# Performance work log

Measured on AMD Instinct MI355X. Metric: run time of the kernel, lower is better.

The kernel has to match this reference:

```python
import jax, jax.numpy as jnp
import numpy as np

N_NODES = 40000
N_EDGES = 640000
D_IN = 128
D_OUT = 128
ALPHA = 0.5   # real-valued complex alpha from init
Q = 0.25      # magnetic potential parameter


def setup_inputs() -> dict:
    key = jax.random.key(0)
    k = jax.random.split(key, 6)
    x = jax.random.normal(k[0], (N_NODES, D_IN), dtype=jnp.float32)
    edge_index = jax.random.randint(k[1], (2, N_EDGES), 0, N_NODES, dtype=jnp.int32)
    W1 = jax.random.normal(k[2], (D_IN, D_OUT), dtype=jnp.float32) * 0.05
    b1 = jax.random.normal(k[3], (D_OUT,), dtype=jnp.float32) * 0.05
    W2 = jax.random.normal(k[4], (D_IN, D_OUT), dtype=jnp.float32) * 0.05
    b2 = jax.random.normal(k[5], (D_OUT,), dtype=jnp.float32) * 0.05
    return {"x": x, "edge_index": edge_index, "W1": W1, "b1": b1, "W2": W2, "b2": b2}


def _magnet_spmm(x, edge_index, q):
    """y = H @ x where H = D_s^{-1/2} (A_s * exp(i*2*pi*q*(A - A^T))) D_s^{-1/2},
    A_s = 0.5*(A + A^T). Returns (y_real, y_imag); x is real (zero imag part)."""
    n = x.shape[0]
    row, col = edge_index[0], edge_index[1]
    e = row.shape[0]
    # detect whether the reverse edge (col,row) exists in the edge set
    keys = row * n + col
    rkeys = col * n + row
    sk = jnp.sort(keys)
    pos = jnp.searchsorted(sk, rkeys)
    has_rev = (pos < e) & (sk[jnp.clip(pos, 0, e - 1)] == rkeys)
    # symmetrize: each directed edge contributes 0.5 in both directions.
    # forward copy carries phase sign +1, reversed copy sign -1; phase is 0
    # when both directions exist (A - A^T = 0 there).
    r_all = jnp.concatenate([row, col])          # [2E]
    c_all = jnp.concatenate([col, row])
    sign = jnp.concatenate([jnp.ones((e,), x.dtype), -jnp.ones((e,), x.dtype)])
    hr = jnp.concatenate([has_rev, has_rev]).astype(x.dtype)
    theta = (2.0 * np.pi * q) * sign * (1.0 - hr)
    half = jnp.asarray(0.5, x.dtype)
    # symmetrized degree: deg[u] = sum_v A_s[u,v]
    deg = jax.ops.segment_sum(jnp.full((2 * e,), 0.5, x.dtype), r_all, num_segments=n)
    dinv = jnp.where(deg > 0, 1.0 / jnp.sqrt(deg), 0.0)
    scale = half * dinv[r_all] * dinv[c_all]
    val_re = scale * jnp.cos(theta)
    val_im = scale * jnp.sin(theta)
    xg = x[c_all]                                # [2E, D] gather
    y_re = jax.ops.segment_sum(val_re[:, None] * xg, r_all, num_segments=n)
    y_im = jax.ops.segment_sum(val_im[:, None] * xg, r_all, num_segments=n)
    return y_re, y_im


def reference(x, edge_index, W1, b1, W2, b2):
    y_re, y_im = _magnet_spmm(x, edge_index, Q)
    # alpha * lin1(y) + (1-alpha) * lin2(y), applied to real and imag parts
    out_re = ALPHA * (y_re @ W1 + b1) + (1.0 - ALPHA) * (y_re @ W2 + b2)
    out_im = ALPHA * (y_im @ W1 + b1) + (1.0 - ALPHA) * (y_im @ W2 + b2)
    return jnp.concatenate([out_re, out_im], axis=1)  # [N, 2*D_OUT]
```

## Files before the change

### kernel.cpp

```cpp
#include <hip/hip_runtime.h>
#include <math.h>

#define N_NODES 40000
#define D 128
#define NEDGE 640000
#define CAP 80

__device__ __forceinline__ unsigned short bf16rn(float f) {
    unsigned u = __float_as_uint(f);
    unsigned r = u + 0x7FFFu + ((u >> 16) & 1u);
    return (unsigned short)(r >> 16);
}

__global__ void init_kernel(int* __restrict__ cursor,
                            const float* __restrict__ W1, const float* __restrict__ b1,
                            const float* __restrict__ W2, const float* __restrict__ b2,
                            float* __restrict__ Wc, float* __restrict__ bc,
                            const float* __restrict__ x, unsigned short* __restrict__ xb) {
    int i = blockIdx.x * blockDim.x + threadIdx.x;
    int stride = gridDim.x * blockDim.x;
    for (int t = i; t < N_NODES; t += stride) cursor[t] = 0;
    for (int t = i; t < D * D; t += stride) Wc[t] = 0.5f * (W1[t] + W2[t]);
    if (i < D) bc[i] = 0.5f * (b1[i] + b2[i]);
    if (xb) {
        for (int t = i; t < N_NODES * D / 4; t += stride) {
            float4 v = ((const float4*)x)[t];
            ushort4 o;
            o.x = bf16rn(v.x); o.y = bf16rn(v.y); o.z = bf16rn(v.z); o.w = bf16rn(v.w);
            ((ushort4*)xb)[t] = o;
        }
    }
}

__global__ void expand_kernel(const int* __restrict__ row, const int* __restrict__ col,
                              int* __restrict__ cursor, unsigned* __restrict__ entries) {
    int e = blockIdx.x * blockDim.x + threadIdx.x;
    if (e >= NEDGE) return;
    int r = row[e], c = col[e];
    int p1 = atomicAdd(&cursor[r], 1);
    if (p1 < CAP) entries[(size_t)r * CAP + p1] = (unsigned)c;
    int p2 = atomicAdd(&cursor[c], 1);
    if (p2 < CAP) entries[(size_t)c * CAP + p2] = (unsigned)r | 0x10000u;
}

template <int USE_BF16>
__global__ __launch_bounds__(256) void fused_kernel(
    const float* __restrict__ x, const unsigned short* __restrict__ xb,
    const unsigned* __restrict__ entries, const int* __restrict__ cursor,
    const float* __restrict__ Wc, const float* __restrict__ bc,
    float* __restrict__ out) {
    __shared__ unsigned rawlds[4][2][CAP];
    __shared__ uint4 slds[4][2][CAP];
    __shared__ float ylds[8][260];

    int tid = threadIdx.x;
    int wave = tid >> 6, half = (tid >> 5) & 1, l = tid & 31;
    int n = wave * 2 + half;
    int u = blockIdx.x * 8 + n;

    int cnt = cursor[u];
    int m = min(cnt, CAP);
    float dinv_u = (cnt > 0) ? rsqrtf(0.5f * (float)cnt) : 0.f;
    const unsigned* eb = entries + (size_t)u * CAP;

    for (int idx = l; idx < m; idx += 32) rawlds[wave][half][idx] = eb[idx];
    __builtin_amdgcn_wave_barrier();

    for (int idx = l; idx < m; idx += 32) {
        unsigned e = rawlds[wave][half][idx];
        unsigned src = e & 0xFFFFu;
        unsigned dir = (e >> 16) & 1u;
        unsigned tgt = src | ((dir ^ 1u) << 16);
        bool rev = false;
        for (int j = 0; j < m; ++j)
            rev |= (rawlds[wave][half][j] == tgt);
        int cs = cursor[src];
        float s = 0.5f * dinv_u * rsqrtf(0.5f * (float)max(cs, 1));
        float sre = 0.f, sim = 0.f;
        if (rev) sre = s;
        else sim = dir ? -s : s;
        slds[wave][half][idx] = make_uint4(src, __float_as_uint(sre),
                                           __float_as_uint(sim), 0u);
    }
    __builtin_amdgcn_wave_barrier();

    float4 accre = make_float4(0.f, 0.f, 0.f, 0.f);
    float4 accim = make_float4(0.f, 0.f, 0.f, 0.f);

    if (USE_BF16) {
        #pragma unroll 8
        for (int i = 0; i < m; ++i) {
            uint4 t = slds[wave][half][i];
            uint2 v = ((const uint2*)(xb + (size_t)t.x * D))[l];
            float fre = __uint_as_float(t.y), fim = __uint_as_float(t.z);
            float v0 = __uint_as_float(v.x << 16);
            float v1 = __uint_as_float(v.x & 0xFFFF0000u);
            float v2 = __uint_as_float(v.y << 16);
            float v3 = __uint_as_float(v.y & 0xFFFF0000u);
            accre.x += fre * v0; accre.y += fre * v1;
            accre.z += fre * v2; accre.w += fre * v3;
            accim.x += fim * v0; accim.y += fim * v1;
            accim.z += fim * v2; accim.w += fim * v3;
        }
    } else {
        #pragma unroll 4
        for (int i = 0; i < m; ++i) {
            uint4 t = slds[wave][half][i];
            float4 v = ((const float4*)(x + (size_t)t.x * D))[l];
            float fre = __uint_as_float(t.y), fim = __uint_as_float(t.z);
            accre.x += fre * v.x; accre.y += fre * v.y;
            accre.z += fre * v.z; accre.w += fre * v.w;
            accim.x += fim * v.x; accim.y += fim * v.y;
            accim.z += fim * v.z; accim.w += fim * v.w;
        }
    }

    *(float4*)&ylds[n][l * 4] = accre;
    *(float4*)&ylds[n][128 + l * 4] = accim;
    __syncthreads();

    int n2 = tid >> 5, c = tid & 31;
    int u2 = blockIdx.x * 8 + n2;
    const float* yb = &ylds[n2][0];
    const float4* Wc4 = (const float4*)Wc;
    float4 ar = make_float4(0.f, 0.f, 0.f, 0.f);
    float4 ai = make_float4(0.f, 0.f, 0.f, 0.f);
    #pragma unroll 4
    for (int k = 0; k < 128; k += 4) {
        float4 yr4 = *(const float4*)&yb[k];
        float4 yi4 = *(const float4*)&yb[128 + k];
        #pragma unroll
        for (int j = 0; j < 4; ++j) {
            float4 w = Wc4[(k + j) * 32 + c];
            float yr = (j == 0) ? yr4.x : (j == 1) ? yr4.y : (j == 2) ? yr4.z : yr4.w;
            float yi = (j == 0) ? yi4.x : (j == 1) ? yi4.y : (j == 2) ? yi4.z : yi4.w;
            ar.x += yr * w.x; ar.y += yr * w.y; ar.z += yr * w.z; ar.w += yr * w.w;
            ai.x += yi * w.x; ai.y += yi * w.y; ai.z += yi * w.z; ai.w += yi * w.w;
        }
    }
    float4 bv = ((const float4*)bc)[c];
    ar.x += bv.x; ar.y += bv.y; ar.z += bv.z; ar.w += bv.w;
    ai.x += bv.x; ai.y += bv.y; ai.z += bv.z; ai.w += bv.w;
    *(float4*)&out[(size_t)u2 * 256 + c * 4] = ar;
    *(float4*)&out[(size_t)u2 * 256 + 128 + c * 4] = ai;
}

extern "C" void kernel_launch(void* const* d_in, const int* in_sizes, int n_in,
                              void* d_out, int out_size, void* d_ws, size_t ws_size,
                              hipStream_t stream) {
    const float* x  = (const float*)d_in[0];
    const int*   ei = (const int*)d_in[1];
    const float* W1 = (const float*)d_in[2];
    const float* b1 = (const float*)d_in[3];
    const float* W2 = (const float*)d_in[4];
    const float* b2 = (const float*)d_in[5];
    float* out = (float*)d_out;
    const int* row = ei;
    const int* col = ei + NEDGE;

    char* ws = (char*)d_ws;
    float*    Wc      = (float*)ws;
    float*    bc      = (float*)(ws + 65536);
    int*      cursor  = (int*)(ws + 66048);
    unsigned* entries = (unsigned*)(ws + 226048);
    const size_t xoff = 13026048;
    const size_t XBB = (size_t)N_NODES * D * 2;

    unsigned short* xb = nullptr;
    bool bf16 = false;
    if (ws_size >= xoff + XBB) {
        xb = (unsigned short*)(ws + xoff);
        bf16 = true;
    }

    init_kernel<<<2048, 256, 0, stream>>>(cursor, W1, b1, W2, b2, Wc, bc, x, xb);
    expand_kernel<<<(NEDGE + 255) / 256, 256, 0, stream>>>(row, col, cursor, entries);
    if (bf16) {
        fused_kernel<1><<<N_NODES / 8, 256, 0, stream>>>(x, xb, entries, cursor, Wc, bc, out);
    } else {
        fused_kernel<0><<<N_NODES / 8, 256, 0, stream>>>(x, xb, entries, cursor, Wc, bc, out);
    }
}
```

Baseline: 216.3 us.

## Merge init, expand and fused stages into one cooperative persistent kernel

Replaces the three kernel launches with a single cooperative kernel that uses grid-wide syncs between the init, edge-expansion and aggregation+GEMM phases. The last phase becomes a persistent loop over node groups. The aim is to remove launch overhead and inter-kernel gaps. In exchange, grid size is capped by occupancy, so the aggregation phase has fewer blocks to hide latency, and grid.sync adds its own cost. It also simplifies the reverse-edge target computation to an XOR.

```diff
diff --git a/kernel.cpp b/kernel.cpp
--- a/kernel.cpp
+++ b/kernel.cpp
@@ -1,15 +1,154 @@
 #include <hip/hip_runtime.h>
+#include <hip/hip_cooperative_groups.h>
 #include <math.h>
+
+namespace cg = cooperative_groups;
 
 #define N_NODES 40000
 #define D 128
 #define NEDGE 640000
 #define CAP 80
+#define NGROUP (N_NODES / 8)
 
 __device__ __forceinline__ unsigned short bf16rn(float f) {
     unsigned u = __float_as_uint(f);
     unsigned r = u + 0x7FFFu + ((u >> 16) & 1u);
     return (unsigned short)(r >> 16);
+}
+
+template <int USE_BF16>
+__global__ __launch_bounds__(256) void mega_kernel(
+    const float* __restrict__ x, unsigned short* __restrict__ xb,
+    const int* __restrict__ row, const int* __restrict__ col,
+    int* __restrict__ cursor, unsigned* __restrict__ entries,
+    const float* __restrict__ W1, const float* __restrict__ b1,
+    const float* __restrict__ W2, const float* __restrict__ b2,
+    float* __restrict__ Wc, float* __restrict__ bc,
+    float* __restrict__ out) {
+    cg::grid_group grid = cg::this_grid();
+    int gtid = blockIdx.x * blockDim.x + threadIdx.x;
+    int gstride = gridDim.x * blockDim.x;
+
+    for (int t = gtid; t < N_NODES; t += gstride) cursor[t] = 0;
+    for (int t = gtid; t < D * D; t += gstride) Wc[t] = 0.5f * (W1[t] + W2[t]);
+    for (int t = gtid; t < D; t += gstride) bc[t] = 0.5f * (b1[t] + b2[t]);
+    if (USE_BF16) {
+        for (int t = gtid; t < N_NODES * D / 4; t += gstride) {
+            float4 v = ((const float4*)x)[t];
+            ushort4 o;
+            o.x = bf16rn(v.x); o.y = bf16rn(v.y); o.z = bf16rn(v.z); o.w = bf16rn(v.w);
+            ((ushort4*)xb)[t] = o;
+        }
+    }
+    grid.sync();
+
+    for (int e = gtid; e < NEDGE; e += gstride) {
+        int r = row[e], c = col[e];
+        int p1 = atomicAdd(&cursor[r], 1);
+        if (p1 < CAP) entries[(size_t)r * CAP + p1] = (unsigned)c;
+        int p2 = atomicAdd(&cursor[c], 1);
+        if (p2 < CAP) entries[(size_t)c * CAP + p2] = (unsigned)r | 0x10000u;
+    }
+    grid.sync();
+
+    __shared__ unsigned rawlds[4][2][CAP];
+    __shared__ uint4 slds[4][2][CAP];
+    __shared__ float ylds[8][260];
+
+    int tid = threadIdx.x;
+    int wave = tid >> 6, half = (tid >> 5) & 1, l = tid & 31;
+    int n = wave * 2 + half;
+
+    for (int g = blockIdx.x; g < NGROUP; g += gridDim.x) {
+        __syncthreads();
+        int u = g * 8 + n;
+
+        int cnt = cursor[u];
+        int m = min(cnt, CAP);
+        float dinv_u = (cnt > 0) ? rsqrtf(0.5f * (float)cnt) : 0.f;
+        const unsigned* eb = entries + (size_t)u * CAP;
+
+        for (int idx = l; idx < m; idx += 32) rawlds[wave][half][idx] = eb[idx];
+        __builtin_amdgcn_wave_barrier();
+
+        for (int idx = l; idx < m; idx += 32) {
+            unsigned e = rawlds[wave][half][idx];
+            unsigned src = e & 0xFFFFu;
+            unsigned dir = (e >> 16) & 1u;
+            unsigned tgt = e ^ 0x10000u;
+            bool rev = false;
+            for (int j = 0; j < m; ++j)
+                rev |= (rawlds[wave][half][j] == tgt);
+            int cs = cursor[src];
+            float s = 0.5f * dinv_u * rsqrtf(0.5f * (float)max(cs, 1));
+            float sre = 0.f, sim = 0.f;
+            if (rev) sre = s;
+            else sim = dir ? -s : s;
+            slds[wave][half][idx] = make_uint4(src, __float_as_uint(sre),
+                                               __float_as_uint(sim), 0u);
+        }
+        __builtin_amdgcn_wave_barrier();
+
+        float4 accre = make_float4(0.f, 0.f, 0.f, 0.f);
+        float4 accim = make_float4(0.f, 0.f, 0.f, 0.f);
+
+        if (USE_BF16) {
+            #pragma unroll 8
+            for (int i = 0; i < m; ++i) {
+                uint4 t = slds[wave][half][i];
+                uint2 v = ((const uint2*)(xb + (size_t)t.x * D))[l];
+                float fre = __uint_as_float(t.y), fim = __uint_as_float(t.z);
+                float v0 = __uint_as_float(v.x << 16);
+                float v1 = __uint_as_float(v.x & 0xFFFF0000u);
+                float v2 = __uint_as_float(v.y << 16);
+                float v3 = __uint_as_float(v.y & 0xFFFF0000u);
+                accre.x += fre * v0; accre.y += fre * v1;
+                accre.z += fre * v2; accre.w += fre * v3;
+                accim.x += fim * v0; accim.y += fim * v1;
+                accim.z += fim * v2; accim.w += fim * v3;
+            }
+        } else {
+            #pragma unroll 4
+            for (int i = 0; i < m; ++i) {
+                uint4 t = slds[wave][half][i];
+                float4 v = ((const float4*)(x + (size_t)t.x * D))[l];
+                float fre = __uint_as_float(t.y), fim = __uint_as_float(t.z);
+                accre.x += fre * v.x; accre.y += fre * v.y;
+                accre.z += fre * v.z; accre.w += fre * v.w;
+                accim.x += fim * v.x; accim.y += fim * v.y;
+                accim.z += fim * v.z; accim.w += fim * v.w;
+            }
+        }
+
+        *(float4*)&ylds[n][l * 4] = accre;
+        *(float4*)&ylds[n][128 + l * 4] = accim;
+        __syncthreads();
+
+        int n2 = tid >> 5, c = tid & 31;
+        int u2 = g * 8 + n2;
+        const float* yb = &ylds[n2][0];
+        const float4* Wc4 = (const float4*)Wc;
+        float4 ar = make_float4(0.f, 0.f, 0.f, 0.f);
+        float4 ai = make_float4(0.f, 0.f, 0.f, 0.f);
+        #pragma unroll 4
+        for (int k = 0; k < 128; k += 4) {
+            float4 yr4 = *(const float4*)&yb[k];
+            float4 yi4 = *(const float4*)&yb[128 + k];
+            #pragma unroll
+            for (int j = 0; j < 4; ++j) {
+                float4 w = Wc4[(k + j) * 32 + c];
+                float yr = (j == 0) ? yr4.x : (j == 1) ? yr4.y : (j == 2) ? yr4.z : yr4.w;
+                float yi = (j == 0) ? yi4.x : (j == 1) ? yi4.y : (j == 2) ? yi4.z : yi4.w;
+                ar.x += yr * w.x; ar.y += yr * w.y; ar.z += yr * w.z; ar.w += yr * w.w;
+                ai.x += yi * w.x; ai.y += yi * w.y; ai.z += yi * w.z; ai.w += yi * w.w;
+            }
+        }
+        float4 bv = ((const float4*)bc)[c];
+        ar.x += bv.x; ar.y += bv.y; ar.z += bv.z; ar.w += bv.w;
+        ai.x += bv.x; ai.y += bv.y; ai.z += bv.z; ai.w += bv.w;
+        *(float4*)&out[(size_t)u2 * 256 + c * 4] = ar;
+        *(float4*)&out[(size_t)u2 * 256 + 128 + c * 4] = ai;
+    }
 }
 
 __global__ void init_kernel(int* __restrict__ cursor,
@@ -70,7 +209,7 @@
         unsigned e = rawlds[wave][half][idx];
         unsigned src = e & 0xFFFFu;
         unsigned dir = (e >> 16) & 1u;
-        unsigned tgt = src | ((dir ^ 1u) << 16);
+        unsigned tgt = e ^ 0x10000u;
         bool rev = false;
         for (int j = 0; j < m; ++j)
             rev |= (rawlds[wave][half][j] == tgt);
@@ -173,11 +312,29 @@
         bf16 = true;
     }
 
-    init_kernel<<<2048, 256, 0, stream>>>(cursor, W1, b1, W2, b2, Wc, bc, x, xb);
-    expand_kernel<<<(NEDGE + 255) / 256, 256, 0, stream>>>(row, col, cursor, entries);
-    if (bf16) {
-        fused_kernel<1><<<N_NODES / 8, 256, 0, stream>>>(x, xb, entries, cursor, Wc, bc, out);
-    } else {
-        fused_kernel<0><<<N_NODES / 8, 256, 0, stream>>>(x, xb, entries, cursor, Wc, bc, out);
-    }
-}
+    const void* fn = bf16 ? reinterpret_cast<const void*>(&mega_kernel<1>)
+                          : reinterpret_cast<const void*>(&mega_kernel<0>);
+    int nb = 0;
+    if (hipOccupancyMaxActiveBlocksPerMultiprocessor(&nb, fn, 256, 0) != hipSuccess || nb <= 0)
+        nb = 4;
+    int grid = nb * 256;
+    if (grid > 2048) grid = 2048;
+
+    void* args[] = {(void*)&x, (void*)&xb, (void*)&row, (void*)&col,
+                    (void*)&cursor, (void*)&entries,
+                    (void*)&W1, (void*)&b1, (void*)&W2, (void*)&b2,
+                    (void*)&Wc, (void*)&bc, (void*)&out};
+    hipError_t err = hipLaunchCooperativeKernel(fn, dim3(grid), dim3(256), args, 0, stream);
+
+    if (err != hipSuccess) {
+        init_kernel<<<2048, 256, 0, stream>>>(cursor, W1, b1, W2, b2, Wc, bc, x, xb);
+        expand_kernel<<<(NEDGE + 255) / 256, 256, 0, stream>>>(row, col, cursor, entries);
+        if (bf16) {
+            fused_kernel<1><<<N_NODES / 8, 256, 0, stream>>>(x, xb, entries, cursor,
+                                                             Wc, bc, out);
+        } else {
+            fused_kernel<0><<<N_NODES / 8, 256, 0, stream>>>(x, xb, entries, cursor,
+                                                             Wc, bc, out);
+        }
+    }
+}
```

After: 382.3 us. 76.7% more time.

## Split adjacency into two-ended 16-bit lists and halve reverse-edge search

Applied to the files above, without the earlier changes.

Uses separate out/in counters so each node's edge slots fill forward for outgoing and backward for incoming edges, which allows 16-bit entries and removes the packed direction bit. The reverse-edge check now scans only the opposite-direction segment rather than the whole list. Per-edge LDS records shrink from 16 to 8 bytes, with the real/imag split rebuilt from a flag bit. The bf16 conversion of x moves from the init kernel into a grid-stride expand kernel, trading more per-edge selects and two cursor reads per neighbour for less memory traffic.

```diff
diff --git a/kernel.cpp b/kernel.cpp
--- a/kernel.cpp
+++ b/kernel.cpp
@@ -12,18 +12,32 @@
     return (unsigned short)(r >> 16);
 }
 
-__global__ void init_kernel(int* __restrict__ cursor,
+__global__ void init_kernel(int* __restrict__ cursorA, int* __restrict__ cursorB,
                             const float* __restrict__ W1, const float* __restrict__ b1,
                             const float* __restrict__ W2, const float* __restrict__ b2,
-                            float* __restrict__ Wc, float* __restrict__ bc,
-                            const float* __restrict__ x, unsigned short* __restrict__ xb) {
+                            float* __restrict__ Wc, float* __restrict__ bc) {
     int i = blockIdx.x * blockDim.x + threadIdx.x;
     int stride = gridDim.x * blockDim.x;
-    for (int t = i; t < N_NODES; t += stride) cursor[t] = 0;
+    for (int t = i; t < N_NODES; t += stride) { cursorA[t] = 0; cursorB[t] = 0; }
     for (int t = i; t < D * D; t += stride) Wc[t] = 0.5f * (W1[t] + W2[t]);
     if (i < D) bc[i] = 0.5f * (b1[i] + b2[i]);
+}
+
+__global__ void expand_kernel(const int* __restrict__ row, const int* __restrict__ col,
+                              int* __restrict__ cursorA, int* __restrict__ cursorB,
+                              unsigned short* __restrict__ entries,
+                              const float* __restrict__ x, unsigned short* __restrict__ xb) {
+    int i = blockIdx.x * blockDim.x + threadIdx.x;
+    int gstride = gridDim.x * blockDim.x;
+    for (int e = i; e < NEDGE; e += gstride) {
+        int r = row[e], c = col[e];
+        int p1 = atomicAdd(&cursorA[r], 1);
+        if (p1 < CAP) entries[(size_t)r * CAP + p1] = (unsigned short)c;
+        int p2 = atomicAdd(&cursorB[c], 1);
+        if (p2 < CAP) entries[(size_t)c * CAP + (CAP - 1 - p2)] = (unsigned short)r;
+    }
     if (xb) {
-        for (int t = i; t < N_NODES * D / 4; t += stride) {
+        for (int t = i; t < N_NODES * D / 4; t += gstride) {
             float4 v = ((const float4*)x)[t];
             ushort4 o;
             o.x = bf16rn(v.x); o.y = bf16rn(v.y); o.z = bf16rn(v.z); o.w = bf16rn(v.w);
@@ -32,25 +46,15 @@
     }
 }
 
-__global__ void expand_kernel(const int* __restrict__ row, const int* __restrict__ col,
-                              int* __restrict__ cursor, unsigned* __restrict__ entries) {
-    int e = blockIdx.x * blockDim.x + threadIdx.x;
-    if (e >= NEDGE) return;
-    int r = row[e], c = col[e];
-    int p1 = atomicAdd(&cursor[r], 1);
-    if (p1 < CAP) entries[(size_t)r * CAP + p1] = (unsigned)c;
-    int p2 = atomicAdd(&cursor[c], 1);
-    if (p2 < CAP) entries[(size_t)c * CAP + p2] = (unsigned)r | 0x10000u;
-}
-
 template <int USE_BF16>
 __global__ __launch_bounds__(256) void fused_kernel(
     const float* __restrict__ x, const unsigned short* __restrict__ xb,
-    const unsigned* __restrict__ entries, const int* __restrict__ cursor,
+    const unsigned short* __restrict__ entries,
+    const int* __restrict__ cursorA, const int* __restrict__ cursorB,
     const float* __restrict__ Wc, const float* __restrict__ bc,
     float* __restrict__ out) {
-    __shared__ unsigned rawlds[4][2][CAP];
-    __shared__ uint4 slds[4][2][CAP];
+    __shared__ unsigned short rawlds[4][2][CAP];
+    __shared__ uint2 slds[4][2][CAP];
     __shared__ float ylds[8][260];
 
     int tid = threadIdx.x;
@@ -58,29 +62,33 @@
     int n = wave * 2 + half;
     int u = blockIdx.x * 8 + n;
 
-    int cnt = cursor[u];
-    int m = min(cnt, CAP);
+    int cA = cursorA[u], cB = cursorB[u];
+    int a = min(cA, CAP);
+    int b = min(cB, CAP - a);
+    int m = a + b;
+    int cnt = cA + cB;
     float dinv_u = (cnt > 0) ? rsqrtf(0.5f * (float)cnt) : 0.f;
-    const unsigned* eb = entries + (size_t)u * CAP;
-
-    for (int idx = l; idx < m; idx += 32) rawlds[wave][half][idx] = eb[idx];
+    const unsigned short* eb = entries + (size_t)u * CAP;
+    int gap = CAP - m;
+
+    for (int t = l; t < m; t += 32)
+        rawlds[wave][half][t] = eb[t < a ? t : t + gap];
     __builtin_amdgcn_wave_barrier();
 
-    for (int idx = l; idx < m; idx += 32) {
-        unsigned e = rawlds[wave][half][idx];
-        unsigned src = e & 0xFFFFu;
-        unsigned dir = (e >> 16) & 1u;
-        unsigned tgt = src | ((dir ^ 1u) << 16);
+    for (int t = l; t < m; t += 32) {
+        unsigned short src = rawlds[wave][half][t];
+        bool d1 = (t >= a);
+        int lo = d1 ? 0 : a, hi = d1 ? a : m;
         bool rev = false;
-        for (int j = 0; j < m; ++j)
-            rev |= (rawlds[wave][half][j] == tgt);
-        int cs = cursor[src];
+        for (int j = lo; j < hi; ++j)
+            rev |= (rawlds[wave][half][j] == src);
+        int cs = cursorA[src] + cursorB[src];
         float s = 0.5f * dinv_u * rsqrtf(0.5f * (float)max(cs, 1));
-        float sre = 0.f, sim = 0.f;
-        if (rev) sre = s;
-        else sim = dir ? -s : s;
-        slds[wave][half][idx] = make_uint4(src, __float_as_uint(sre),
-                                           __float_as_uint(sim), 0u);
+        unsigned flag = 0u;
+        float sval;
+        if (rev) { sval = s; flag = 0x10000u; }
+        else     { sval = d1 ? -s : s; }
+        slds[wave][half][t] = make_uint2((unsigned)src | flag, __float_as_uint(sval));
     }
     __builtin_amdgcn_wave_barrier();
 
@@ -90,9 +98,13 @@
     if (USE_BF16) {
         #pragma unroll 8
         for (int i = 0; i < m; ++i) {
-            uint4 t = slds[wave][half][i];
-            uint2 v = ((const uint2*)(xb + (size_t)t.x * D))[l];
-            float fre = __uint_as_float(t.y), fim = __uint_as_float(t.z);
+            uint2 t = slds[wave][half][i];
+            unsigned src = t.x & 0xFFFFu;
+            float s = __uint_as_float(t.y);
+            bool isre = (t.x & 0x10000u) != 0u;
+            float fre = isre ? s : 0.f;
+            float fim = isre ? 0.f : s;
+            uint2 v = ((const uint2*)(xb + (size_t)src * D))[l];
             float v0 = __uint_as_float(v.x << 16);
             float v1 = __uint_as_float(v.x & 0xFFFF0000u);
             float v2 = __uint_as_float(v.y << 16);
@@ -105,9 +117,13 @@
     } else {
         #pragma unroll 4
         for (int i = 0; i < m; ++i) {
-            uint4 t = slds[wave][half][i];
-            float4 v = ((const float4*)(x + (size_t)t.x * D))[l];
-            float fre = __uint_as_float(t.y), fim = __uint_as_float(t.z);
+            uint2 t = slds[wave][half][i];
+            unsigned src = t.x & 0xFFFFu;
+            float s = __uint_as_float(t.y);
+            bool isre = (t.x & 0x10000u) != 0u;
+            float fre = isre ? s : 0.f;
+            float fim = isre ? 0.f : s;
+            float4 v = ((const float4*)(x + (size_t)src * D))[l];
             accre.x += fre * v.x; accre.y += fre * v.y;
             accre.z += fre * v.z; accre.w += fre * v.w;
             accim.x += fim * v.x; accim.y += fim * v.y;
@@ -159,11 +175,12 @@
     const int* col = ei + NEDGE;
 
     char* ws = (char*)d_ws;
-    float*    Wc      = (float*)ws;
-    float*    bc      = (float*)(ws + 65536);
-    int*      cursor  = (int*)(ws + 66048);
-    unsigned* entries = (unsigned*)(ws + 226048);
-    const size_t xoff = 13026048;
+    float*          Wc      = (float*)ws;
+    float*          bc      = (float*)(ws + 65536);
+    int*            cursorA = (int*)(ws + 66048);
+    int*            cursorB = (int*)(ws + 226048);
+    unsigned short* entries = (unsigned short*)(ws + 386048);
+    const size_t xoff = 6786048;
     const size_t XBB = (size_t)N_NODES * D * 2;
 
     unsigned short* xb = nullptr;
@@ -173,11 +190,13 @@
         bf16 = true;
     }
 
-    init_kernel<<<2048, 256, 0, stream>>>(cursor, W1, b1, W2, b2, Wc, bc, x, xb);
-    expand_kernel<<<(NEDGE + 255) / 256, 256, 0, stream>>>(row, col, cursor, entries);
+    init_kernel<<<512, 256, 0, stream>>>(cursorA, cursorB, W1, b1, W2, b2, Wc, bc);
+    expand_kernel<<<2500, 256, 0, stream>>>(row, col, cursorA, cursorB, entries, x, xb);
     if (bf16) {
-        fused_kernel<1><<<N_NODES / 8, 256, 0, stream>>>(x, xb, entries, cursor, Wc, bc, out);
+        fused_kernel<1><<<N_NODES / 8, 256, 0, stream>>>(x, xb, entries, cursorA, cursorB,
+                                                         Wc, bc, out);
     } else {
-        fused_kernel<0><<<N_NODES / 8, 256, 0, stream>>>(x, xb, entries, cursor, Wc, bc, out);
-    }
-}
+        fused_kernel<0><<<N_NODES / 8, 256, 0, stream>>>(x, xb, entries, cursorA, cursorB,
+                                                         Wc, bc, out);
+    }
+}
```

Result: faster. 196.3 us (-9.3%).
